# Optimization experiments

Measured on AMD Instinct MI355X. Metric: run time of the kernel, lower is better.

Reference implementation:

```python
import jax, jax.numpy as jnp
import numpy as np

B, T, V, TS, H = 128, 64, 1024, 64, 512  # batch, max visits, visit_size, time_size, hidden_size


def setup_inputs() -> dict:
    key = jax.random.key(0)
    ks = jax.random.split(key, 9)
    s = 1.0 / np.sqrt(H)  # torch RNN-cell init scale
    return {
        "visit_emb": jax.random.normal(ks[0], (B, T, V), jnp.float32),
        "intervals": jax.random.uniform(ks[1], (B, T), jnp.float32),
        "W_time": jax.random.uniform(ks[2], (TS, 1), jnp.float32, -1.0, 1.0),
        "b_time": jax.random.uniform(ks[3], (TS,), jnp.float32, -1.0, 1.0),
        "W_ih": jax.random.uniform(ks[4], (3 * H, V + TS), jnp.float32, -s, s),
        "W_hh": jax.random.uniform(ks[5], (3 * H, H), jnp.float32, -s, s),
        "b_ih": jax.random.uniform(ks[6], (3 * H,), jnp.float32, -s, s),
        "b_hh": jax.random.uniform(ks[7], (3 * H,), jnp.float32, -s, s),
        "lens": jax.random.randint(ks[8], (B,), 0, T, dtype=jnp.int32),
    }


def reference(visit_emb, intervals, W_time, b_time, W_ih, W_hh, b_ih, b_hh, lens):
    b, t, _ = visit_emb.shape
    h_dim = W_hh.shape[1]
    # time-aware embedding: Linear(1, time_size) applied to each scalar interval
    t_emb = intervals[..., None] * W_time[:, 0] + b_time              # [B, T, TS]
    x = jnp.concatenate([visit_emb, t_emb], axis=-1)                  # [B, T, V+TS]
    # precompute the input-side gate projection as one big GEMM
    xg = jnp.einsum("bti,gi->btg", x, W_ih) + b_ih                    # [B, T, 3H]
    mask = jnp.arange(t)[None, :] < lens[:, None]                     # [B, T]

    xg_flat = xg.reshape(b * t, 3 * h_dim)
    m_flat = mask.reshape(b * t)

    def step(h, inp):
        xgi, m = inp
        gh = W_hh @ h + b_hh                                          # [3H]
        r = jax.nn.sigmoid(xgi[:h_dim] + gh[:h_dim])
        z = jax.nn.sigmoid(xgi[h_dim:2 * h_dim] + gh[h_dim:2 * h_dim])
        n = jnp.tanh(xgi[2 * h_dim:] + r * gh[2 * h_dim:])
        h_new = (1.0 - z) * n + z * h
        h = jnp.where(m, h_new, h)  # skip padded timesteps (t >= len)
        return h, h

    h0 = jnp.zeros((h_dim,), visit_emb.dtype)
    # NOTE: hidden is NOT reset between samples in the original module; the
    # state flows continuously over the whole batch, matching a single scan.
    _, hs = jax.lax.scan(step, h0, (xg_flat, m_flat))
    out = hs.reshape(b, t, h_dim)[:, -1, :]                           # hidden after each sample
    return out
```

## Files before the change

### kernel.cpp

```cpp
#include <hip/hip_runtime.h>
#include <stdint.h>

#define B_   128
#define T_   64
#define V_   1024
#define TS_  64
#define H_   512
#define K_   (V_ + TS_)


__device__ __forceinline__ float sigmoidf_(float x) {
    return 1.0f / (1.0f + __expf(-x));
}
__device__ __forceinline__ float tanhf_(float x) {
    x = fminf(fmaxf(x, -15.0f), 15.0f);
    const float e = __expf(2.0f * x);
    return (e - 1.0f) / (e + 1.0f);
}
__device__ __forceinline__ uint32_t bf16_rn_(float f) {
    uint32_t u = __float_as_uint(f);
    u += 0x7FFFu + ((u >> 16) & 1u);
    return u >> 16;
}
__device__ __forceinline__ float bf16_to_f32_(uint32_t b) {
    return __uint_as_float(b << 16);
}

template <int CTRL, int RM, int BM>
__device__ __forceinline__ float dpp_add_(float a) {
    const int x = __builtin_amdgcn_update_dpp(
        0, __float_as_int(a), CTRL, RM, BM, true);
    return a + __int_as_float(x);
}
__device__ __forceinline__ float wave_sum_(float a) {
    a = dpp_add_<0x111, 0xF, 0xF>(a);
    a = dpp_add_<0x112, 0xF, 0xF>(a);
    a = dpp_add_<0x114, 0xF, 0xE>(a);
    a = dpp_add_<0x118, 0xF, 0xC>(a);
    a = dpp_add_<0x142, 0xA, 0xF>(a);
    a = dpp_add_<0x143, 0xC, 0xF>(a);
    return __int_as_float(__builtin_amdgcn_readlane(__float_as_int(a), 63));
}

__global__ __launch_bounds__(256, 1) void gru_fused(
    const float* __restrict__ visit_emb, const float* __restrict__ intervals,
    const float* __restrict__ W_time, const float* __restrict__ b_time,
    const float* __restrict__ W_ih, const float* __restrict__ W_hh,
    const float* __restrict__ b_ih, const float* __restrict__ b_hh,
    const int* __restrict__ lens,
    uint64_t* h_buf ,
    float* __restrict__ out)
{
    const int lane = threadIdx.x & 63;
    const int wave = threadIdx.x >> 6;
    const int q    = blockIdx.x * 4 + wave;
    const int j0   = q * 2;
    const int j1   = j0 + 1;

    __shared__ float2 hs2[256];
    float* hs = (float*)hs2;

    float wr0[8], wr1[8], wz0[8], wz1[8], wn0[8], wn1[8];
    #pragma unroll
    for (int u = 0; u < 8; ++u) {
        const int k = lane + 64 * u;
        wr0[u] = W_hh[(size_t)j0 * H_ + k];
        wr1[u] = W_hh[(size_t)j1 * H_ + k];
        wz0[u] = W_hh[(size_t)(H_ + j0) * H_ + k];
        wz1[u] = W_hh[(size_t)(H_ + j1) * H_ + k];
        wn0[u] = W_hh[(size_t)(2 * H_ + j0) * H_ + k];
        wn1[u] = W_hh[(size_t)(2 * H_ + j1) * H_ + k];
    }
    float ir0[17], ir1[17], iz0[17], iz1[17], in0[17], in1[17];
    #pragma unroll
    for (int u = 0; u < 16; ++u) {
        const int k = lane + 64 * u;
        ir0[u] = W_ih[(size_t)j0 * K_ + k];
        ir1[u] = W_ih[(size_t)j1 * K_ + k];
        iz0[u] = W_ih[(size_t)(H_ + j0) * K_ + k];
        iz1[u] = W_ih[(size_t)(H_ + j1) * K_ + k];
        in0[u] = W_ih[(size_t)(2 * H_ + j0) * K_ + k];
        in1[u] = W_ih[(size_t)(2 * H_ + j1) * K_ + k];
    }
    ir0[16] = W_ih[(size_t)j0 * K_ + V_ + lane];
    ir1[16] = W_ih[(size_t)j1 * K_ + V_ + lane];
    iz0[16] = W_ih[(size_t)(H_ + j0) * K_ + V_ + lane];
    iz1[16] = W_ih[(size_t)(H_ + j1) * K_ + V_ + lane];
    in0[16] = W_ih[(size_t)(2 * H_ + j0) * K_ + V_ + lane];
    in1[16] = W_ih[(size_t)(2 * H_ + j1) * K_ + V_ + lane];

    const float wt = W_time[lane];
    const float bt = b_time[lane];

    const float bir0 = b_ih[j0],          bir1 = b_ih[j1];
    const float biz0 = b_ih[H_ + j0],     biz1 = b_ih[H_ + j1];
    const float bin0 = b_ih[2 * H_ + j0], bin1 = b_ih[2 * H_ + j1];
    const float bhr0 = b_hh[j0],          bhr1 = b_hh[j1];
    const float bhz0 = b_hh[H_ + j0],     bhz1 = b_hh[H_ + j1];
    const float bhn0 = b_hh[2 * H_ + j0], bhn1 = b_hh[2 * H_ + j1];

    float hj0 = 0.0f, hj1 = 0.0f;
    uint32_t ver  = 1;
    uint32_t dead = 0;

    if (lane == 0)
        __hip_atomic_store(&h_buf[(ver & 1) * 256 + q], (uint64_t)ver << 32,
                           __ATOMIC_RELAXED, __HIP_MEMORY_SCOPE_AGENT);

    float xv[16];
    float iv = 0.0f;

    for (int b = 0; b < B_; ++b) {
        const int L = lens[b];
        if (L > 0) {
            iv = intervals[b * T_];
            const float* vrow = visit_emb + (size_t)(b * T_) * V_;
            #pragma unroll
            for (int u = 0; u < 16; ++u) xv[u] = vrow[lane + 64 * u];
        }
        for (int t = 0; t < L; ++t) {
            const uint64_t* src = h_buf + (ver & 1) * 256;
            uint64_t w[4];
            if (wave == 0) {
                #pragma unroll
                for (int u = 0; u < 4; ++u)
                    w[u] = __hip_atomic_load(&src[lane + 64 * u],
                                             __ATOMIC_RELAXED,
                                             __HIP_MEMORY_SCOPE_AGENT);
            }

            const float xt = fmaf(iv, wt, bt);
            float ar0 = ir0[16] * xt, ar1 = ir1[16] * xt;
            float az0 = iz0[16] * xt, az1 = iz1[16] * xt;
            float xn0 = in0[16] * xt, xn1 = in1[16] * xt;
            #pragma unroll
            for (int u = 0; u < 16; ++u) {
                ar0 = fmaf(ir0[u], xv[u], ar0);
                ar1 = fmaf(ir1[u], xv[u], ar1);
                az0 = fmaf(iz0[u], xv[u], az0);
                az1 = fmaf(iz1[u], xv[u], az1);
                xn0 = fmaf(in0[u], xv[u], xn0);
                xn1 = fmaf(in1[u], xv[u], xn1);
            }
            if (t + 1 < L) {
                iv = intervals[b * T_ + t + 1];
                const float* vrow = visit_emb + (size_t)(b * T_ + t + 1) * V_;
                #pragma unroll
                for (int u = 0; u < 16; ++u) xv[u] = vrow[lane + 64 * u];
            }

            if (wave == 0) {
                if (!dead) {
                    bool ok = true;
                    #pragma unroll
                    for (int u = 0; u < 4; ++u)
                        ok = ok && ((uint32_t)(w[u] >> 32) == ver);
                    uint32_t tries = 0;
                    while (!__all(ok)) {
                        if (++tries > (1u << 21)) { dead = 1; break; }
                        ok = true;
                        #pragma unroll
                        for (int u = 0; u < 4; ++u) {
                            w[u] = __hip_atomic_load(&src[lane + 64 * u],
                                                     __ATOMIC_RELAXED,
                                                     __HIP_MEMORY_SCOPE_AGENT);
                            ok = ok && ((uint32_t)(w[u] >> 32) == ver);
                        }
                    }
                }
                #pragma unroll
                for (int u = 0; u < 4; ++u) {
                    const uint32_t d = (uint32_t)w[u];
                    hs2[lane + 64 * u] =
                        make_float2(bf16_to_f32_(d & 0xFFFFu),
                                    bf16_to_f32_(d >> 16));
                }
            }
            __syncthreads();

            float h[8];
            #pragma unroll
            for (int u = 0; u < 8; ++u) h[u] = hs[lane + 64 * u];

            float hn0 = 0.0f, hn1 = 0.0f;
            #pragma unroll
            for (int u = 0; u < 8; ++u) {
                ar0 = fmaf(wr0[u], h[u], ar0);
                ar1 = fmaf(wr1[u], h[u], ar1);
                az0 = fmaf(wz0[u], h[u], az0);
                az1 = fmaf(wz1[u], h[u], az1);
                hn0 = fmaf(wn0[u], h[u], hn0);
                hn1 = fmaf(wn1[u], h[u], hn1);
            }

            const float sr0 = wave_sum_(ar0), sr1 = wave_sum_(ar1);
            const float sz0 = wave_sum_(az0), sz1 = wave_sum_(az1);
            const float sx0 = wave_sum_(xn0), sx1 = wave_sum_(xn1);
            const float sh0 = wave_sum_(hn0), sh1 = wave_sum_(hn1);

            const float r0 = sigmoidf_(sr0 + bir0 + bhr0);
            const float r1 = sigmoidf_(sr1 + bir1 + bhr1);
            const float z0 = sigmoidf_(sz0 + biz0 + bhz0);
            const float z1 = sigmoidf_(sz1 + biz1 + bhz1);
            const float n0 = tanhf_(sx0 + bin0 + r0 * (sh0 + bhn0));
            const float n1 = tanhf_(sx1 + bin1 + r1 * (sh1 + bhn1));
            hj0 = (1.0f - z0) * n0 + z0 * hj0;
            hj1 = (1.0f - z1) * n1 + z1 * hj1;

            ++ver;
            if (lane == 0) {
                const uint32_t packed =
                    bf16_rn_(hj0) | (bf16_rn_(hj1) << 16);
                __hip_atomic_store(&h_buf[(ver & 1) * 256 + q],
                    ((uint64_t)ver << 32) | (uint64_t)packed,
                    __ATOMIC_RELAXED, __HIP_MEMORY_SCOPE_AGENT);
            }
        }
        if (lane < 2) out[b * H_ + j0 + lane] = (lane == 0) ? hj0 : hj1;
    }
}

extern "C" void kernel_launch(void* const* d_in, const int* in_sizes, int n_in,
                              void* d_out, int out_size, void* d_ws, size_t ws_size,
                              hipStream_t stream)
{
    const float* visit_emb = (const float*)d_in[0];
    const float* intervals = (const float*)d_in[1];
    const float* W_time    = (const float*)d_in[2];
    const float* b_time    = (const float*)d_in[3];
    const float* W_ih      = (const float*)d_in[4];
    const float* W_hh      = (const float*)d_in[5];
    const float* b_ih      = (const float*)d_in[6];
    const float* b_hh      = (const float*)d_in[7];
    const int*   lens      = (const int*)d_in[8];
    float*       out       = (float*)d_out;

    uint64_t* h_buf = (uint64_t*)d_ws;

    gru_fused<<<64, 256, 0, stream>>>(visit_emb, intervals, W_time, b_time,
                                      W_ih, W_hh, b_ih, b_hh, lens, h_buf, out);
}
```

Before: 7.419 ms.

## Poll hidden state in every wave and drop LDS broadcast and barrier

Each wave now reads the packed bf16 hidden-state words from global memory directly, instead of wave 0 reading them and passing them through shared memory with a __syncthreads. The W_hh register layout is permuted so each lane's eight h values line up with the two halves of its four packed words. Polling alternates between two in-flight load sets so a fresh load is always outstanding while the previous one is checked. The aim is to take the LDS round trip and the block barrier off the serial per-timestep critical path, at the cost of four times more global polling traffic on the shared buffer.

```diff
diff --git a/kernel.cpp b/kernel.cpp
--- a/kernel.cpp
+++ b/kernel.cpp
@@ -41,6 +41,22 @@
     a = dpp_add_<0x143, 0xC, 0xF>(a);
     return __int_as_float(__builtin_amdgcn_readlane(__float_as_int(a), 63));
 }
+
+#define LOADW(d0, d1, d2, d3)                                                 \
+    do {                                                                      \
+        d0 = __hip_atomic_load(&src[lane],       __ATOMIC_RELAXED,            \
+                               __HIP_MEMORY_SCOPE_AGENT);                     \
+        d1 = __hip_atomic_load(&src[lane + 64],  __ATOMIC_RELAXED,            \
+                               __HIP_MEMORY_SCOPE_AGENT);                     \
+        d2 = __hip_atomic_load(&src[lane + 128], __ATOMIC_RELAXED,            \
+                               __HIP_MEMORY_SCOPE_AGENT);                     \
+        d3 = __hip_atomic_load(&src[lane + 192], __ATOMIC_RELAXED,            \
+                               __HIP_MEMORY_SCOPE_AGENT);                     \
+    } while (0)
+
+#define TAGOK4(d0, d1, d2, d3)                                                \
+    (((uint32_t)((d0) >> 32) == ver) && ((uint32_t)((d1) >> 32) == ver) &&    \
+     ((uint32_t)((d2) >> 32) == ver) && ((uint32_t)((d3) >> 32) == ver))
 
 __global__ __launch_bounds__(256, 1) void gru_fused(
     const float* __restrict__ visit_emb, const float* __restrict__ intervals,
@@ -57,20 +73,20 @@
     const int j0   = q * 2;
     const int j1   = j0 + 1;
 
-    __shared__ float2 hs2[256];
-    float* hs = (float*)hs2;
-
     float wr0[8], wr1[8], wz0[8], wz1[8], wn0[8], wn1[8];
     #pragma unroll
-    for (int u = 0; u < 8; ++u) {
-        const int k = lane + 64 * u;
-        wr0[u] = W_hh[(size_t)j0 * H_ + k];
-        wr1[u] = W_hh[(size_t)j1 * H_ + k];
-        wz0[u] = W_hh[(size_t)(H_ + j0) * H_ + k];
-        wz1[u] = W_hh[(size_t)(H_ + j1) * H_ + k];
-        wn0[u] = W_hh[(size_t)(2 * H_ + j0) * H_ + k];
-        wn1[u] = W_hh[(size_t)(2 * H_ + j1) * H_ + k];
-    }
+    for (int u = 0; u < 4; ++u)
+        #pragma unroll
+        for (int s = 0; s < 2; ++s) {
+            const int k = 2 * lane + 128 * u + s;
+            const int v = 2 * u + s;
+            wr0[v] = W_hh[(size_t)j0 * H_ + k];
+            wr1[v] = W_hh[(size_t)j1 * H_ + k];
+            wz0[v] = W_hh[(size_t)(H_ + j0) * H_ + k];
+            wz1[v] = W_hh[(size_t)(H_ + j1) * H_ + k];
+            wn0[v] = W_hh[(size_t)(2 * H_ + j0) * H_ + k];
+            wn1[v] = W_hh[(size_t)(2 * H_ + j1) * H_ + k];
+        }
     float ir0[17], ir1[17], iz0[17], iz1[17], in0[17], in1[17];
     #pragma unroll
     for (int u = 0; u < 16; ++u) {
@@ -120,14 +136,9 @@
         }
         for (int t = 0; t < L; ++t) {
             const uint64_t* src = h_buf + (ver & 1) * 256;
-            uint64_t w[4];
-            if (wave == 0) {
-                #pragma unroll
-                for (int u = 0; u < 4; ++u)
-                    w[u] = __hip_atomic_load(&src[lane + 64 * u],
-                                             __ATOMIC_RELAXED,
-                                             __HIP_MEMORY_SCOPE_AGENT);
-            }
+            uint64_t a0, a1, a2, a3, c0, c1, c2, c3;
+
+            LOADW(a0, a1, a2, a3);
 
             const float xt = fmaf(iv, wt, bt);
             float ar0 = ir0[16] * xt, ar1 = ir1[16] * xt;
@@ -149,48 +160,47 @@
                 for (int u = 0; u < 16; ++u) xv[u] = vrow[lane + 64 * u];
             }
 
-            if (wave == 0) {
-                if (!dead) {
-                    bool ok = true;
-                    #pragma unroll
-                    for (int u = 0; u < 4; ++u)
-                        ok = ok && ((uint32_t)(w[u] >> 32) == ver);
-                    uint32_t tries = 0;
-                    while (!__all(ok)) {
-                        if (++tries > (1u << 21)) { dead = 1; break; }
-                        ok = true;
-                        #pragma unroll
-                        for (int u = 0; u < 4; ++u) {
-                            w[u] = __hip_atomic_load(&src[lane + 64 * u],
-                                                     __ATOMIC_RELAXED,
-                                                     __HIP_MEMORY_SCOPE_AGENT);
-                            ok = ok && ((uint32_t)(w[u] >> 32) == ver);
-                        }
+            uint64_t w0, w1, w2, w3;
+            if (!dead) {
+                LOADW(c0, c1, c2, c3);
+                uint32_t tries = 0;
+                for (;;) {
+                    if (__all(TAGOK4(a0, a1, a2, a3))) {
+                        w0 = a0; w1 = a1; w2 = a2; w3 = a3; break;
                     }
+                    LOADW(a0, a1, a2, a3);
+                    if (++tries > (1u << 21)) {
+                        dead = 1;
+                        w0 = c0; w1 = c1; w2 = c2; w3 = c3; break;
+                    }
+                    if (__all(TAGOK4(c0, c1, c2, c3))) {
+                        w0 = c0; w1 = c1; w2 = c2; w3 = c3; break;
+                    }
+                    LOADW(c0, c1, c2, c3);
                 }
-                #pragma unroll
-                for (int u = 0; u < 4; ++u) {
-                    const uint32_t d = (uint32_t)w[u];
-                    hs2[lane + 64 * u] =
-                        make_float2(bf16_to_f32_(d & 0xFFFFu),
-                                    bf16_to_f32_(d >> 16));
-                }
-            }
-            __syncthreads();
+            } else {
+                w0 = a0; w1 = a1; w2 = a2; w3 = a3;
+            }
 
             float h[8];
-            #pragma unroll
-            for (int u = 0; u < 8; ++u) h[u] = hs[lane + 64 * u];
+            {
+                const uint32_t d0 = (uint32_t)w0, d1 = (uint32_t)w1;
+                const uint32_t d2 = (uint32_t)w2, d3 = (uint32_t)w3;
+                h[0] = bf16_to_f32_(d0 & 0xFFFFu); h[1] = bf16_to_f32_(d0 >> 16);
+                h[2] = bf16_to_f32_(d1 & 0xFFFFu); h[3] = bf16_to_f32_(d1 >> 16);
+                h[4] = bf16_to_f32_(d2 & 0xFFFFu); h[5] = bf16_to_f32_(d2 >> 16);
+                h[6] = bf16_to_f32_(d3 & 0xFFFFu); h[7] = bf16_to_f32_(d3 >> 16);
+            }
 
             float hn0 = 0.0f, hn1 = 0.0f;
             #pragma unroll
-            for (int u = 0; u < 8; ++u) {
-                ar0 = fmaf(wr0[u], h[u], ar0);
-                ar1 = fmaf(wr1[u], h[u], ar1);
-                az0 = fmaf(wz0[u], h[u], az0);
-                az1 = fmaf(wz1[u], h[u], az1);
-                hn0 = fmaf(wn0[u], h[u], hn0);
-                hn1 = fmaf(wn1[u], h[u], hn1);
+            for (int v = 0; v < 8; ++v) {
+                ar0 = fmaf(wr0[v], h[v], ar0);
+                ar1 = fmaf(wr1[v], h[v], ar1);
+                az0 = fmaf(wz0[v], h[v], az0);
+                az1 = fmaf(wz1[v], h[v], az1);
+                hn0 = fmaf(wn0[v], h[v], hn0);
+                hn1 = fmaf(wn1[v], h[v], hn1);
             }
 
             const float sr0 = wave_sum_(ar0), sr1 = wave_sum_(ar1);
@@ -209,8 +219,7 @@
 
             ++ver;
             if (lane == 0) {
-                const uint32_t packed =
-                    bf16_rn_(hj0) | (bf16_rn_(hj1) << 16);
+                const uint32_t packed = bf16_rn_(hj0) | (bf16_rn_(hj1) << 16);
                 __hip_atomic_store(&h_buf[(ver & 1) * 256 + q],
                     ((uint64_t)ver << 32) | (uint64_t)packed,
                     __ATOMIC_RELAXED, __HIP_MEMORY_SCOPE_AGENT);
```

New measurement: 16.35 ms. 120% more time.
